# Performance work log

Measured on AMD Instinct MI355X. Metric: run time of the kernel, lower is better.

## Reference

```python
import jax, jax.numpy as jnp
import numpy as np

WINDOW = 3
RATIO = 5


def _box_filter(x, win):
    """Depthwise 3D box (mean) filter, 'same' padding, per channel.
    x: [N, C, D, H, W] -> [N, C, D, H, W]
    Matches torch conv3d with ones([1,1,w,w,w])/w^3 applied per channel.
    """
    c = x.shape[1]
    k = jnp.ones((c, 1, win, win, win), x.dtype) / (win ** 3)
    pad = win // 2
    return jax.lax.conv_general_dilated(
        x, k,
        window_strides=(1, 1, 1),
        padding=[(pad, pad)] * 3,
        dimension_numbers=('NCDHW', 'OIDHW', 'NCDHW'),
        feature_group_count=c,
    )


def setup_inputs() -> dict:
    key = jax.random.key(0)
    k1, k2 = jax.random.split(key)
    y_pred = jax.random.normal(k1, (1, 3, 192, 192, 192), dtype=jnp.float32)
    y_true = jax.random.uniform(k2, (1, 1, 192, 192, 192), dtype=jnp.float32)
    return {"y_pred": y_pred, "y_true": y_true}


def reference(y_pred, y_true):
    # Finite differences (abs), each [1, 3, D-1, H-1, W-1]
    base = y_pred[:, :, :-1, :-1, :-1]
    dy = jnp.abs(y_pred[:, :, 1:, :-1, :-1] - base)
    dx = jnp.abs(y_pred[:, :, :-1, 1:, :-1] - base)
    dz = jnp.abs(y_pred[:, :, :-1, :-1, 1:] - base)

    # 9 box-filtered single-channel maps == 3 depthwise box filters
    fx = _box_filter(dx, WINDOW)
    fy = _box_filter(dy, WINDOW)
    fz = _box_filter(dz, WINDOW)
    dxdx, dxdy, dxdz = fx[:, 1:2], fy[:, 1:2], fz[:, 1:2]
    dydx, dydy, dydz = fx[:, 0:1], fy[:, 0:1], fz[:, 0:1]
    dzdx, dzdy, dzdz = fx[:, 2:3], fy[:, 2:3], fz[:, 2:3]

    # Neo-Hookean invariants
    det_1 = (dxdx + 1) * ((dydy + 1) * (dzdz + 1) - dydz * dzdy)
    det_2 = -dxdy * (dydx * (dzdz + 1) - dydz * dzdx)
    det_3 = dxdz * (dydx * dzdy - (dydy + 1) * dzdx)
    J = det_1 + det_2 + det_3

    Tr = ((dxdx + 1) ** 2 + dxdy ** 2 + dxdz ** 2
          + dydx ** 2 + (dydy + 1) ** 2 + dydz ** 2
          + dzdx ** 2 + dzdy ** 2 + (dzdz + 1) ** 2)

    # mode == 'exp'
    stretch = Tr * jnp.exp(-J + 1) - 3
    vol_change = (J - 1) ** 2

    # Faithful replication of the sequential mu/lambda normalization in torch:
    mu = 1.0
    lam = mu * RATIO
    mu = mu / (mu + lam)          # 1/6
    lam = lam / (mu + lam)        # 30/31 (uses updated mu, as in source)

    U = mu / 2 * stretch + lam / 2 * vol_change
    return jnp.mean(U)
```

## Files before the change

### kernel.cpp

```cpp
#include <hip/hip_runtime.h>
#include <math.h>

#define DIM 192
#define OD  191
#define VOL 7077888
#define TW  14
#define TH  16
#define CD  24
#define NBW 14
#define NBH 12
#define NCH 8

typedef float    f4 __attribute__((ext_vector_type(4)));
typedef _Float16 h8 __attribute__((ext_vector_type(8)));
typedef _Float16 h2 __attribute__((ext_vector_type(2)));

template<int CTRL>
__device__ __forceinline__ int dppi(int x) {
    return __builtin_amdgcn_update_dpp(0, x, CTRL, 0xF, 0xF, true);
}

union U8 { h8 v; int i[4]; };
union U2 { h2 v; int i; };

__device__ __forceinline__ void wsum3(h8& a, h2& b) {
    U8 ua, s1, s2;
    ua.v = a;
    #pragma unroll
    for (int k = 0; k < 4; ++k) {
        s1.i[k] = dppi<0x101>(ua.i[k]);
        s2.i[k] = dppi<0x111>(ua.i[k]);
    }
    a = ua.v + s1.v + s2.v;
    U2 ub, t1, t2;
    ub.v = b;
    t1.i = dppi<0x101>(ub.i);
    t2.i = dppi<0x111>(ub.i);
    b = ub.v + t1.v + t2.v;
}

__device__ __forceinline__ void make_diff(const f4 c, const f4 cw, const f4 ch, const f4 cd,
                                          h8& va, h2& vb) {
    const float hx  = fabsf(ch.x - c.x), hy  = fabsf(ch.y - c.y), hz  = fabsf(ch.z - c.z);
    const float dx_ = fabsf(cd.x - c.x), dy_ = fabsf(cd.y - c.y), dz_ = fabsf(cd.z - c.z);
    const float wx  = fabsf(cw.x - c.x), wy  = fabsf(cw.y - c.y), wz  = fabsf(cw.z - c.z);
    va = (h8){(_Float16)hx,  (_Float16)hy,  (_Float16)hz,
              (_Float16)dx_, (_Float16)dy_, (_Float16)dz_,
              (_Float16)wx,  (_Float16)wy};
    vb = (h2){(_Float16)wz, (_Float16)0.f};
}

__global__ __launch_bounds__(256, 6)
void nh_fused_kernel(const float* __restrict__ P, float* __restrict__ out) {
    const int tid = threadIdx.x;
    const int tx  = tid & 15;
    const int ty  = tid >> 4;
    const int w0  = blockIdx.x * TW;
    const int h0  = blockIdx.y * TH;
    const int ds  = blockIdx.z * CD;
    const int de  = min(ds + CD, OD);

    __shared__ f4 sraw[2][19][18];
    __shared__ h8 sW[18][16];
    __shared__ h2 sWB[18][16];
    __shared__ float wsum[4];

    const bool valid = (tx < TW) && (w0 + tx < OD) && (h0 + ty < OD);

    h8 a0 = (h8)0, a1 = (h8)0, a2 = (h8)0;
    h2 b0 = (h2)0, b1 = (h2)0, b2 = (h2)0;
    f4 cur = (f4)0, prev = (f4)0;
    float acc = 0.f;

    for (int t = ds - 1; t <= de + 1; ++t) {
        const int cb = t & 1, pb = cb ^ 1;

        if (t >= 0 && t < DIM) {
            {
                const int hp = h0 - 1 + ty;
                const int wp = w0 - 1 + tx;
                f4 r = (f4)0;
                if (hp >= 0 && hp < DIM && wp >= 0 && wp < DIM) {
                    const size_t base = ((size_t)t * DIM + (size_t)hp) * DIM + (size_t)wp;
                    r.x = P[base];
                    r.y = P[base + VOL];
                    r.z = P[base + 2 * VOL];
                }
                sraw[cb][ty][tx] = r;
                cur = r;
            }
            if (tid < 67) {
                int hh, ww;
                if (tid < 16) { hh = tid; ww = 16; }
                else { const int l = tid - 16; const int q = l / 17; hh = 16 + q; ww = l - 17 * q; }
                const int hp = h0 - 1 + hh;
                const int wp = w0 - 1 + ww;
                f4 r = (f4)0;
                if (hp >= 0 && hp < DIM && wp >= 0 && wp < DIM) {
                    const size_t base = ((size_t)t * DIM + (size_t)hp) * DIM + (size_t)wp;
                    r.x = P[base];
                    r.y = P[base + VOL];
                    r.z = P[base + 2 * VOL];
                }
                sraw[cb][hh][ww] = r;
            }
        } else {
            cur = (f4)0;
        }
        __syncthreads();

        const int p = t - 1;
        const bool built = (p >= 0) && (p < OD) && (t >= ds);

        {
            h8 sa = (h8)0; h2 sb = (h2)0;
            if (built) {
                const int hp = h0 - 1 + ty;
                const int wp = w0 - 1 + tx;
                h8 va = (h8)0; h2 vb = (h2)0;
                if (hp >= 0 && hp < OD && wp >= 0 && wp < OD) {
                    const f4 c  = prev;
                    const f4 cw = sraw[pb][ty][tx + 1];
                    const f4 ch = sraw[pb][ty + 1][tx];
                    const f4 cd = cur;
                    make_diff(c, cw, ch, cd, va, vb);
                }
                wsum3(va, vb);
                sa = va; sb = vb;
            }
            sW[ty][tx] = sa; sWB[ty][tx] = sb;
        }
        if (tid < 32) {
            const int rr   = 16 + (tid >> 4);
            const int lane = tid & 15;
            h8 sa = (h8)0; h2 sb = (h2)0;
            if (built) {
                const int hp = h0 - 1 + rr;
                const int wp = w0 - 1 + lane;
                h8 va = (h8)0; h2 vb = (h2)0;
                if (hp >= 0 && hp < OD && wp >= 0 && wp < OD) {
                    const f4 c  = sraw[pb][rr][lane];
                    const f4 cw = sraw[pb][rr][lane + 1];
                    const f4 ch = sraw[pb][rr + 1][lane];
                    const f4 cd = sraw[cb][rr][lane];
                    make_diff(c, cw, ch, cd, va, vb);
                }
                wsum3(va, vb);
                sa = va; sb = vb;
            }
            sW[rr][lane] = sa; sWB[rr][lane] = sb;
        }
        __syncthreads();

        a0 = a1; a1 = a2; b0 = b1; b1 = b2;
        {
            const int cc = (tx + 1) & 15;
            a2 = sW[ty][cc] + sW[ty + 1][cc] + sW[ty + 2][cc];
            b2 = sWB[ty][cc] + sWB[ty + 1][cc] + sWB[ty + 2][cc];
        }

        const int d = t - 2;
        if (valid && d >= ds && d < de) {
            const h8 FA = a0 + a1 + a2;
            const h2 FB = b0 + b1 + b2;
            const float inv27 = 1.f / 27.f;
            const float dydx = (float)FA[0] * inv27, dxdx = (float)FA[1] * inv27, dzdx = (float)FA[2] * inv27;
            const float dydy = (float)FA[3] * inv27, dxdy = (float)FA[4] * inv27, dzdy = (float)FA[5] * inv27;
            const float dydz = (float)FA[6] * inv27, dxdz = (float)FA[7] * inv27, dzdz = (float)FB[0] * inv27;
            const float a = dxdx + 1.f, e = dydy + 1.f, iN = dzdz + 1.f;
            const float J = a * (e * iN - dydz * dzdy)
                          - dxdy * (dydx * iN - dydz * dzdx)
                          + dxdz * (dydx * dzdy - e * dzdx);
            const float Tr = a * a + dxdy * dxdy + dxdz * dxdz
                           + dydx * dydx + e * e + dydz * dydz
                           + dzdx * dzdx + dzdy * dzdy + iN * iN;
            const float stretch = Tr * expf(1.f - J) - 3.f;
            const float vol = (J - 1.f) * (J - 1.f);
            acc += 0.0833333358f * stretch + 0.4838709677f * vol;
        }

        prev = cur;
    }

    acc *= (1.f / 6967871.f);

    #pragma unroll
    for (int off = 32; off > 0; off >>= 1) acc += __shfl_down(acc, off, 64);
    if ((tid & 63) == 0) wsum[tid >> 6] = acc;
    __syncthreads();
    if (tid == 0) {
        atomicAdd(out, wsum[0] + wsum[1] + wsum[2] + wsum[3]);
    }
}

extern "C" void kernel_launch(void* const* d_in, const int* in_sizes, int n_in,
                              void* d_out, int out_size, void* d_ws, size_t ws_size,
                              hipStream_t stream) {
    const float* y_pred = (const float*)d_in[0];
    float* out = (float*)d_out;

    hipMemsetAsync(out, 0, sizeof(float), stream);

    dim3 grid(NBW, NBH, NCH);
    nh_fused_kernel<<<grid, 256, 0, stream>>>(y_pred, out);
}
```

Before: 183.6 us.

## Prefetch next depth plane into registers and double-buffer shared tiles to drop a barrier

Each thread now loads the next depth plane's three channels into registers one iteration early, so global loads overlap the current plane's compute. The shared raw and window-sum tiles are double-buffered, which removes one __syncthreads per depth step. The halo-thread mapping is simplified with precomputed bounds and base offsets. Depth chunking also shrinks from 24 to 16 planes, giving more blocks, and launch bounds rise to 7, at the cost of more redundant halo-plane loads and extra register pressure.

New measurement: 173.6 us. 5.4% less time.

```diff
diff --git a/kernel.cpp b/kernel.cpp
--- a/kernel.cpp
+++ b/kernel.cpp
@@ -3,13 +3,14 @@
 
 #define DIM 192
 #define OD  191
+#define PLANE 36864
 #define VOL 7077888
 #define TW  14
 #define TH  16
-#define CD  24
+#define CD  16
 #define NBW 14
 #define NBH 12
-#define NCH 8
+#define NCH 12
 
 typedef float    f4 __attribute__((ext_vector_type(4)));
 typedef _Float16 h8 __attribute__((ext_vector_type(8)));
@@ -50,7 +51,17 @@
     vb = (h2){(_Float16)wz, (_Float16)0.f};
 }
 
-__global__ __launch_bounds__(256, 6)
+__device__ __forceinline__ f4 ld3(const float* __restrict__ P, int idx, bool ok) {
+    f4 r = (f4)0;
+    if (ok) {
+        r.x = P[idx];
+        r.y = P[idx + VOL];
+        r.z = P[idx + 2 * VOL];
+    }
+    return r;
+}
+
+__global__ __launch_bounds__(256, 7)
 void nh_fused_kernel(const float* __restrict__ P, float* __restrict__ out) {
     const int tid = threadIdx.x;
     const int tx  = tid & 15;
@@ -61,102 +72,99 @@
     const int de  = min(ds + CD, OD);
 
     __shared__ f4 sraw[2][19][18];
-    __shared__ h8 sW[18][16];
-    __shared__ h2 sWB[18][16];
+    __shared__ h8 sW[2][18][16];
+    __shared__ h2 sWB[2][18][16];
     __shared__ float wsum[4];
+
+    const int hp_p = h0 - 1 + ty;
+    const int wp_p = w0 - 1 + tx;
+    const bool in_raw_p  = (hp_p >= 0) & (hp_p < DIM) & (wp_p >= 0) & (wp_p < DIM);
+    const bool in_diff_p = (hp_p >= 0) & (hp_p < OD)  & (wp_p >= 0) & (wp_p < OD);
+    const int base_p = hp_p * DIM + wp_p;
+
+    int hh_l, ww_l;
+    if (tid < 48) { hh_l = 16 + (tid >> 4); ww_l = tid & 15; }
+    else          { hh_l = tid - 48;        ww_l = 16; }
+    const bool has_l = (tid < 67);
+    const int hp_l = h0 - 1 + hh_l;
+    const int wp_l = w0 - 1 + ww_l;
+    const bool in_raw_l  = has_l & (hp_l >= 0) & (hp_l < DIM) & (wp_l >= 0) & (wp_l < DIM);
+    const bool in_diff_l = (tid < 32) & (hp_l >= 0) & (hp_l < OD) & (wp_l >= 0) & (wp_l < OD);
+    const int base_l = hp_l * DIM + wp_l;
 
     const bool valid = (tx < TW) && (w0 + tx < OD) && (h0 + ty < OD);
 
     h8 a0 = (h8)0, a1 = (h8)0, a2 = (h8)0;
     h2 b0 = (h2)0, b1 = (h2)0, b2 = (h2)0;
-    f4 cur = (f4)0, prev = (f4)0;
+    f4 cur_p = (f4)0, prev_p = (f4)0;
+    f4 cur_l = (f4)0, prev_l = (f4)0;
     float acc = 0.f;
+
+    {
+        const int t0 = ds - 1;
+        if (t0 >= 0) {
+            cur_p = ld3(P, t0 * PLANE + base_p, in_raw_p);
+            cur_l = ld3(P, t0 * PLANE + base_l, in_raw_l);
+        }
+    }
 
     for (int t = ds - 1; t <= de + 1; ++t) {
         const int cb = t & 1, pb = cb ^ 1;
 
-        if (t >= 0 && t < DIM) {
-            {
-                const int hp = h0 - 1 + ty;
-                const int wp = w0 - 1 + tx;
-                f4 r = (f4)0;
-                if (hp >= 0 && hp < DIM && wp >= 0 && wp < DIM) {
-                    const size_t base = ((size_t)t * DIM + (size_t)hp) * DIM + (size_t)wp;
-                    r.x = P[base];
-                    r.y = P[base + VOL];
-                    r.z = P[base + 2 * VOL];
-                }
-                sraw[cb][ty][tx] = r;
-                cur = r;
+        f4 nxt_p = (f4)0, nxt_l = (f4)0;
+        {
+            const int tn = t + 1;
+            if ((tn < DIM) & (tn <= de + 1)) {
+                nxt_p = ld3(P, tn * PLANE + base_p, in_raw_p);
+                nxt_l = ld3(P, tn * PLANE + base_l, in_raw_l);
             }
-            if (tid < 67) {
-                int hh, ww;
-                if (tid < 16) { hh = tid; ww = 16; }
-                else { const int l = tid - 16; const int q = l / 17; hh = 16 + q; ww = l - 17 * q; }
-                const int hp = h0 - 1 + hh;
-                const int wp = w0 - 1 + ww;
-                f4 r = (f4)0;
-                if (hp >= 0 && hp < DIM && wp >= 0 && wp < DIM) {
-                    const size_t base = ((size_t)t * DIM + (size_t)hp) * DIM + (size_t)wp;
-                    r.x = P[base];
-                    r.y = P[base + VOL];
-                    r.z = P[base + 2 * VOL];
-                }
-                sraw[cb][hh][ww] = r;
-            }
-        } else {
-            cur = (f4)0;
-        }
-        __syncthreads();
-
-        const int p = t - 1;
-        const bool built = (p >= 0) && (p < OD) && (t >= ds);
+        }
+
+        sraw[cb][ty][tx] = cur_p;
+        if (has_l) sraw[cb][hh_l][ww_l] = cur_l;
+
+        const bool built = (t >= ds) & (t - 1 >= 0) & (t - 1 < OD);
 
         {
             h8 sa = (h8)0; h2 sb = (h2)0;
             if (built) {
-                const int hp = h0 - 1 + ty;
-                const int wp = w0 - 1 + tx;
                 h8 va = (h8)0; h2 vb = (h2)0;
-                if (hp >= 0 && hp < OD && wp >= 0 && wp < OD) {
-                    const f4 c  = prev;
+                if (in_diff_p) {
+                    const f4 c  = prev_p;
                     const f4 cw = sraw[pb][ty][tx + 1];
                     const f4 ch = sraw[pb][ty + 1][tx];
-                    const f4 cd = cur;
+                    const f4 cd = cur_p;
                     make_diff(c, cw, ch, cd, va, vb);
                 }
                 wsum3(va, vb);
                 sa = va; sb = vb;
             }
-            sW[ty][tx] = sa; sWB[ty][tx] = sb;
+            sW[cb][ty][tx] = sa; sWB[cb][ty][tx] = sb;
         }
         if (tid < 32) {
-            const int rr   = 16 + (tid >> 4);
-            const int lane = tid & 15;
             h8 sa = (h8)0; h2 sb = (h2)0;
             if (built) {
-                const int hp = h0 - 1 + rr;
-                const int wp = w0 - 1 + lane;
                 h8 va = (h8)0; h2 vb = (h2)0;
-                if (hp >= 0 && hp < OD && wp >= 0 && wp < OD) {
-                    const f4 c  = sraw[pb][rr][lane];
-                    const f4 cw = sraw[pb][rr][lane + 1];
-                    const f4 ch = sraw[pb][rr + 1][lane];
-                    const f4 cd = sraw[cb][rr][lane];
+                if (in_diff_l) {
+                    const f4 c  = prev_l;
+                    const f4 cw = sraw[pb][hh_l][ww_l + 1];
+                    const f4 ch = sraw[pb][hh_l + 1][ww_l];
+                    const f4 cd = cur_l;
                     make_diff(c, cw, ch, cd, va, vb);
                 }
                 wsum3(va, vb);
                 sa = va; sb = vb;
             }
-            sW[rr][lane] = sa; sWB[rr][lane] = sb;
-        }
+            sW[cb][hh_l][ww_l] = sa; sWB[cb][hh_l][ww_l] = sb;
+        }
+
         __syncthreads();
 
         a0 = a1; a1 = a2; b0 = b1; b1 = b2;
         {
             const int cc = (tx + 1) & 15;
-            a2 = sW[ty][cc] + sW[ty + 1][cc] + sW[ty + 2][cc];
-            b2 = sWB[ty][cc] + sWB[ty + 1][cc] + sWB[ty + 2][cc];
+            a2 = sW[cb][ty][cc] + sW[cb][ty + 1][cc] + sW[cb][ty + 2][cc];
+            b2 = sWB[cb][ty][cc] + sWB[cb][ty + 1][cc] + sWB[cb][ty + 2][cc];
         }
 
         const int d = t - 2;
@@ -179,7 +187,8 @@
             acc += 0.0833333358f * stretch + 0.4838709677f * vol;
         }
 
-        prev = cur;
+        prev_p = cur_p; cur_p = nxt_p;
+        prev_l = cur_l; cur_l = nxt_l;
     }
 
     acc *= (1.f / 6967871.f);
```
